# Optimization experiments

Measured on AMD Instinct MI355X. Metric: run time of the kernel, lower is better.

Reference implementation:

```python
import jax, jax.numpy as jnp
import numpy as np

SEGMENT_LENGTHS = (2048, 4096, 8192)
DILATION_RATES = (1, 2, 4)
NUM_HEADS = 12
EMBED_DIM = 768
B, N = 2, 8192


def setup_inputs() -> dict:
    key = jax.random.key(0)
    ks = jax.random.split(key, 11)
    E = EMBED_DIM
    return {
        "query": jax.random.normal(ks[0], (B, N, E), jnp.float32),
        "key": jax.random.normal(ks[1], (B, N, E), jnp.float32),
        "value": jax.random.normal(ks[2], (B, N, E), jnp.float32),
        "Wq": jax.random.normal(ks[3], (E, E), jnp.float32) * (E ** -0.5),
        "bq": jax.random.normal(ks[4], (E,), jnp.float32) * 0.02,
        "Wk": jax.random.normal(ks[5], (E, E), jnp.float32) * (E ** -0.5),
        "bk": jax.random.normal(ks[6], (E,), jnp.float32) * 0.02,
        "Wv": jax.random.normal(ks[7], (E, E), jnp.float32) * (E ** -0.5),
        "bv": jax.random.normal(ks[8], (E,), jnp.float32) * 0.02,
        "Wo": jax.random.normal(ks[9], (E, E), jnp.float32) * (E ** -0.5),
        "bo": jax.random.normal(ks[10], (E,), jnp.float32) * 0.02,
    }


def _dilated_attention(q, k, v):
    # q, k, v: [b, n, h, d]
    b, n, h, d = q.shape
    num_groups = len(DILATION_RATES)
    g = h // num_groups  # heads per dilation group
    scale = float(1.0 / np.sqrt(d))  # xformers default softmax scale
    out = jnp.zeros_like(q)
    for i, (r, s) in enumerate(zip(DILATION_RATES, SEGMENT_LENGTHS)):
        off = i % r
        hmin, hmax = i * g, (i + 1) * g
        nseg = n // s
        # gather: [b, nseg, s/r, g, d]
        qg = q.reshape(b, nseg, s, h, d)[:, :, off::r, hmin:hmax, :]
        kg = k.reshape(b, nseg, s, h, d)[:, :, off::r, hmin:hmax, :]
        vg = v.reshape(b, nseg, s, h, d)[:, :, off::r, hmin:hmax, :]
        scores = jnp.einsum("bnqhd,bnkhd->bnhqk", qg, kg) * scale
        attn = jax.nn.softmax(scores, axis=-1)
        x = jnp.einsum("bnhqk,bnkhd->bnqhd", attn, vg)
        out = (
            out.reshape(b, nseg, s, h, d)
            .at[:, :, off::r, hmin:hmax, :]
            .add(x)
            .reshape(b, n, h, d)
        )
    # faithful to original: normalize by sum over the sequence dimension
    return out / jnp.sum(out, axis=1, keepdims=True)


def reference(query, key, value, Wq, bq, Wk, bk, Wv, bv, Wo, bo):
    b, n, e = query.shape
    h = NUM_HEADS
    d = e // h
    q = (query @ Wq.T + bq).reshape(b, n, h, d)
    k = (key @ Wk.T + bk).reshape(b, n, h, d)
    v = (value @ Wv.T + bv).reshape(b, n, h, d)
    x = _dilated_attention(q, k, v)
    x = x.reshape(b, n, e)
    return x @ Wo.T + bo
```

## Files before the change

kernel.cpp:

```cpp
#include <hip/hip_runtime.h>
#include <hip/hip_bf16.h>
#include <cmath>
#include <cstdint>

#define B_ 2
#define N_ 8192
#define H_ 12
#define D_ 64
#define E_ 768
#define M_ (B_*N_)

typedef __attribute__((ext_vector_type(8))) short short8;
typedef __attribute__((ext_vector_type(4))) short short4v;
typedef __attribute__((ext_vector_type(4))) float float4v;

__device__ inline short f2b(float f) {
  union { float f; unsigned u; } x; x.f = f;
  unsigned r = (x.u + 0x7fffu + ((x.u >> 16) & 1u)) >> 16;
  return (short)r;
}
__device__ inline float b2f(short s) {
  union { unsigned u; float f; } x; x.u = ((unsigned)(unsigned short)s) << 16;
  return x.f;
}
__device__ inline void split2(float f, short& h, short& l) {
  h = f2b(f);
  l = f2b(f - b2f(h));
}
__device__ inline unsigned pack_trunc(float a, float b) {
  return (__float_as_uint(b) & 0xffff0000u) | (__float_as_uint(a) >> 16);
}

#define MFMA(a, b, c) __builtin_amdgcn_mfma_f32_16x16x32_bf16((a), (b), (c), 0, 0, 0)

#if __has_builtin(__builtin_amdgcn_mfma_f32_16x16x16_bf16)
#define MFMA16(a, b, c) __builtin_amdgcn_mfma_f32_16x16x16_bf16((a), (b), (c), 0, 0, 0)
#elif __has_builtin(__builtin_amdgcn_mfma_f32_16x16x16bf16_1k)
#define MFMA16(a, b, c) __builtin_amdgcn_mfma_f32_16x16x16bf16_1k((a), (b), (c), 0, 0, 0)
#else
__device__ inline float4v mfma16_asm(short4v a, short4v b, float4v c) {
  float4v d = c;
  asm volatile("v_mfma_f32_16x16x16_bf16 %0, %1, %2, %0"
               : "+v"(d) : "v"(a), "v"(b));
  return d;
}
#define MFMA16(a, b, c) mfma16_asm((a), (b), (c))
#endif

#define GLOAD_LDS16(g, l) \
  __builtin_amdgcn_global_load_lds((const __attribute__((address_space(1))) void*)(g), \
      (__attribute__((address_space(3))) void*)(l), 16, 0, 0)

__global__ __launch_bounds__(256) void split_kernel(const float* __restrict__ src,
    short* __restrict__ hi, short* __restrict__ lo, int count4)
{
  int i = blockIdx.x * 256 + threadIdx.x;
  if (i >= count4) return;
  float4v t = ((const float4v*)src)[i];
  short4v h4, l4; short hh, ll;
  split2(t.x, hh, ll); h4.x = hh; l4.x = ll;
  split2(t.y, hh, ll); h4.y = hh; l4.y = ll;
  split2(t.z, hh, ll); h4.z = hh; l4.z = ll;
  split2(t.w, hh, ll); h4.w = hh; l4.w = ll;
  ((short4v*)hi)[i] = h4;
  ((short4v*)lo)[i] = l4;
}

__global__ __launch_bounds__(256) void split_w4(
    const float* __restrict__ w0, const float* __restrict__ w1,
    const float* __restrict__ w2, const float* __restrict__ w3,
    short* __restrict__ planes)
{
  int which = blockIdx.y;
  const float* src = which == 0 ? w0 : which == 1 ? w1 : which == 2 ? w2 : w3;
  short* hi = planes + (size_t)(2 * which) * (E_ * E_);
  short* lo = planes + (size_t)(2 * which + 1) * (E_ * E_);
  int i = blockIdx.x * 256 + threadIdx.x;
  if (i >= E_ * E_ / 4) return;
  float4v t = ((const float4v*)src)[i];
  short4v h4, l4; short hh, ll;
  split2(t.x, hh, ll); h4.x = hh; l4.x = ll;
  split2(t.y, hh, ll); h4.y = hh; l4.y = ll;
  split2(t.z, hh, ll); h4.z = hh; l4.z = ll;
  split2(t.w, hh, ll); h4.w = hh; l4.w = ll;
  ((short4v*)hi)[i] = h4;
  ((short4v*)lo)[i] = l4;
}

__global__ __launch_bounds__(256) void inv_kernel(const float* __restrict__ sums,
    float* __restrict__ inv)
{
  int i = blockIdx.x * 256 + threadIdx.x;
  if (i < B_ * E_) inv[i] = 1.0f / sums[i];
}

__global__ __launch_bounds__(256) void prep_out(const float* __restrict__ attn,
    const float* __restrict__ inv, short* __restrict__ xnh, short* __restrict__ xnl)
{
  size_t e4 = ((size_t)blockIdx.x * 256 + threadIdx.x) * 4;
  int e = (int)(e4 % E_);
  int b = (int)(e4 / ((size_t)E_ * N_));
  float4v a = *(const float4v*)(attn + e4);
  float4v iv = *(const float4v*)(inv + (size_t)b * E_ + e);
  a *= iv;
  short4v h4, l4; short hh, ll;
  split2(a.x, hh, ll); h4.x = hh; l4.x = ll;
  split2(a.y, hh, ll); h4.y = hh; l4.y = ll;
  split2(a.z, hh, ll); h4.z = hh; l4.z = ll;
  split2(a.w, hh, ll); h4.w = hh; l4.w = ll;
  *(short4v*)&xnh[e4] = h4;
  *(short4v*)&xnl[e4] = l4;
}

template<bool OUT_PAIR>
__global__ __launch_bounds__(256) void gemm_dma(
    const short* __restrict__ Ah, const short* __restrict__ Al,
    const short* __restrict__ Wh, const short* __restrict__ Wl,
    const float* __restrict__ bias, void* __restrict__ OutH, short* __restrict__ OutL,
    float oscale)
{
  __shared__ short Ash[4096], Asl[4096], Wsh[4096], Wsl[4096];
  const int tid = threadIdx.x;
  const int m0 = blockIdx.y * 128;
  const int n0 = blockIdx.x * 128;
  const int w = tid >> 6, lane = tid & 63, quad = lane >> 4, l16 = lane & 15;
  const int wr = w >> 1, wc = w & 1;
  const int cq = (l16 >> 1) & 3;
  const int dmarow = lane >> 2;
  const int dmacc = (((lane & 3) ^ ((lane >> 3) & 3))) * 8;

  float4v acc[4][4];
#pragma unroll
  for (int a = 0; a < 4; ++a)
#pragma unroll
    for (int c = 0; c < 4; ++c) acc[a][c] = (float4v)0.0f;

  for (int kt = 0; kt < 24; ++kt) {
    const int k0 = kt * 32;
#pragma unroll
    for (int i = 0; i < 2; ++i) {
      int c = w * 2 + i;
      int ldso = c * 512 + lane * 8;
      size_t ga = (size_t)(m0 + c * 16 + dmarow) * E_ + k0 + dmacc;
      size_t gw = (size_t)(n0 + c * 16 + dmarow) * E_ + k0 + dmacc;
      GLOAD_LDS16(Ah + ga, &Ash[ldso]);
      GLOAD_LDS16(Al + ga, &Asl[ldso]);
      GLOAD_LDS16(Wh + gw, &Wsh[ldso]);
      GLOAD_LDS16(Wl + gw, &Wsl[ldso]);
    }
    __syncthreads();

    short8 afh[4], afl[4], bfh[4], bfl[4];
#pragma unroll
    for (int rt = 0; rt < 4; ++rt) {
      int ao = (wr * 64 + rt * 16 + l16) * 32 + (quad ^ cq) * 8;
      afh[rt] = *(const short8*)&Ash[ao];
      afl[rt] = *(const short8*)&Asl[ao];
      int wo = (wc * 64 + rt * 16 + l16) * 32 + (quad ^ cq) * 8;
      bfh[rt] = *(const short8*)&Wsh[wo];
      bfl[rt] = *(const short8*)&Wsl[wo];
    }
#pragma unroll
    for (int rt = 0; rt < 4; ++rt)
#pragma unroll
      for (int ct = 0; ct < 4; ++ct) {
        float4v a = acc[rt][ct];
        a = MFMA(afh[rt], bfh[ct], a);
        a = MFMA(afh[rt], bfl[ct], a);
        a = MFMA(afl[rt], bfh[ct], a);
        acc[rt][ct] = a;
      }
    __syncthreads();
  }

#pragma unroll
  for (int ct = 0; ct < 4; ++ct) {
    int n = n0 + wc * 64 + ct * 16 + l16;
    float bv = bias[n];
#pragma unroll
    for (int rt = 0; rt < 4; ++rt) {
#pragma unroll
      for (int i = 0; i < 4; ++i) {
        int m = m0 + wr * 64 + rt * 16 + quad * 4 + i;
        float v = (acc[rt][ct][i] + bv) * oscale;
        if constexpr (OUT_PAIR) {
          short hh, ll; split2(v, hh, ll);
          ((short*)OutH)[(size_t)m * E_ + n] = hh;
          OutL[(size_t)m * E_ + n] = ll;
        } else {
          ((float*)OutH)[(size_t)m * E_ + n] = v;
        }
      }
    }
  }
}

__device__ __host__ inline int hoff_of(int g, int hg) {
  return g == 0 ? hg * 8192 : (g == 1 ? 32768 + hg * 4096 : 49152 + hg * 2048);
}

__global__ __launch_bounds__(256) void transpose_v(const short* __restrict__ vh,
    const short* __restrict__ vl, short* __restrict__ vgh, short* __restrict__ vgl)
{
  __shared__ short Lh[64 * 68], Ll[64 * 68];
  int bid = blockIdx.x;
  int b = 0;
  if (bid >= 896) { b = 1; bid -= 896; }
  int g, hg, tile;
  if (bid < 512)      { g = 0; hg = bid >> 7; tile = bid & 127; }
  else if (bid < 768) { g = 1; hg = (bid - 512) >> 6; tile = (bid - 512) & 63; }
  else                { g = 2; hg = (bid - 768) >> 5; tile = (bid - 768) & 31; }
  const int h = g * 4 + hg, r = 1 << g, off = g;
  const int ext = 8192 >> g;
  const int jj0 = tile * 64, seg = jj0 >> 11, j0 = jj0 & 2047;
  const int n0 = seg * (2048 << g) + off + j0 * r;
  const int tid = threadIdx.x;

#pragma unroll
  for (int p = 0; p < 2; ++p) {
    int c = tid + p * 256;
    int jr = c >> 3, c8 = (c & 7) * 8;
    size_t gsrc = ((size_t)(b * N_ + n0 + jr * r) * H_ + h) * D_ + c8;
    *(short8*)&Lh[jr * 68 + c8] = *(const short8*)(vh + gsrc);
    *(short8*)&Ll[jr * 68 + c8] = *(const short8*)(vl + gsrc);
  }
  __syncthreads();
  size_t basebh = ((size_t)b * 57344 + hoff_of(g, hg)) * 64;
#pragma unroll
  for (int p = 0; p < 2; ++p) {
    int c = tid + p * 256;
    int dd = c >> 3, jc = (c & 7) * 8;
    short8 oh, ol;
#pragma unroll
    for (int u = 0; u < 8; ++u) {
      oh[u] = Lh[(jc + u) * 68 + dd];
      ol[u] = Ll[(jc + u) * 68 + dd];
    }
    size_t gdst = basebh + (size_t)dd * ext + jj0 + jc;
    *(short8*)(vgh + gdst) = oh;
    *(short8*)(vgl + gdst) = ol;
  }
}

__global__ __launch_bounds__(256, 4) void attn_kernel(
    const short* __restrict__ qh, const short* __restrict__ ql,
    const short* __restrict__ kh, const short* __restrict__ kl,
    const short* __restrict__ vgh, const short* __restrict__ vgl,
    float* __restrict__ attn_out, float* __restrict__ sums)
{
  __shared__ __align__(16) short Ksh[2][32 * 72], Ksl[2][32 * 72];
  __shared__ __align__(16) short Vth[2][64 * 40], Vtl[2][64 * 40];

  int bid = (blockIdx.x & 7) * 112 + (blockIdx.x >> 3);
  int g, t;
  if (bid < 512)      { g = 0; t = bid; }
  else if (bid < 768) { g = 1; t = bid - 512; }
  else                { g = 2; t = bid - 768; }
  const int qtile = t & 15; t >>= 4;
  const int hg = t & 3; t >>= 2;
  const int nseg = 4 >> g;
  const int seg = t & (nseg - 1);
  const int b = t / nseg;
  const int r = 1 << g;
  const int off = g;
  const int h = g * 4 + hg;
  const int segbase = seg * (2048 << g);
  const int ext = 8192 >> g;

  const int tid = threadIdx.x;
  const int w = tid >> 6, lane = tid & 63, quad = lane >> 4, l16 = lane & 15;

  const size_t vbase = ((size_t)b * 57344 + hoff_of(g, hg)) * 64 + (size_t)seg * 2048;

  if (g > 0) {
#pragma unroll
    for (int res0 = 1; res0 < 4; ++res0) {
      if (res0 >= r) break;
      int res = (off + res0) & (r - 1);
      for (int c = 0; c < 8; ++c) {
        int idx = tid + c * 256;
        int jl = idx >> 4, d0 = (idx & 15) * 4;
        int pos = segbase + res + (qtile * 128 + jl) * r;
        *(float4v*)(attn_out + ((size_t)(b * N_ + pos) * H_ + h) * D_ + d0) = (float4v)0.f;
      }
    }
  }

  short8 qfh[2][2], qfl[2][2];
#pragma unroll
  for (int qt = 0; qt < 2; ++qt) {
    int j = qtile * 128 + w * 32 + qt * 16 + l16;
    int pos = segbase + off + j * r;
    size_t base = ((size_t)(b * N_ + pos) * H_ + h) * D_;
#pragma unroll
    for (int ks = 0; ks < 2; ++ks) {
      qfh[qt][ks] = *(const short8*)(qh + base + ks * 32 + quad * 8);
      qfl[qt][ks] = *(const short8*)(ql + base + ks * 32 + quad * 8);
    }
  }

  const int srow = tid >> 3, sc8 = (tid & 7) * 8;
  const int sdd = tid >> 2, skvc = (tid & 3) * 8;
  size_t gbK = ((size_t)(b * N_ + segbase + off + srow * r) * H_ + h) * D_ + sc8;
  const size_t stepK = (size_t)32 * r * (H_ * D_);
  size_t gbV = vbase + (size_t)sdd * ext + skvc;

  short8 rkh, rkl, rvh, rvl;
#define LOADT(tt) do { \
    size_t ka_ = gbK + (size_t)(tt) * stepK; \
    size_t va_ = gbV + (size_t)(tt) * 32; \
    rkh = *(const short8*)(kh + ka_); rkl = *(const short8*)(kl + ka_); \
    rvh = *(const short8*)(vgh + va_); rvl = *(const short8*)(vgl + va_); \
  } while (0)
#define WRITET(cc) do { \
    *(short8*)&Ksh[cc][srow * 72 + sc8] = rkh; \
    *(short8*)&Ksl[cc][srow * 72 + sc8] = rkl; \
    *(short8*)&Vth[cc][sdd * 40 + skvc] = rvh; \
    *(short8*)&Vtl[cc][sdd * 40 + skvc] = rvl; \
  } while (0)

  float4v o[4][2];
  float mrow[2], lrow[2];
#pragma unroll
  for (int dt = 0; dt < 4; ++dt)
#pragma unroll
    for (int qt = 0; qt < 2; ++qt) o[dt][qt] = (float4v)0.0f;
  mrow[0] = mrow[1] = -INFINITY;
  lrow[0] = lrow[1] = 0.f;

  LOADT(0);
  WRITET(0);
  LOADT(1);
  __syncthreads();
  int cur = 0;

  for (int kt = 0; kt < 64; ++kt) {
    WRITET(cur ^ 1);
    LOADT((kt + 2) & 63);

    const short* Kc_h = Ksh[cur]; const short* Kc_l = Ksl[cur];
    const short* Vc_h = Vth[cur]; const short* Vc_l = Vtl[cur];

    float4v sc[2][2];
    __builtin_amdgcn_s_setprio(1);
#pragma unroll
    for (int kvt = 0; kvt < 2; ++kvt) {
      const int kb = (kvt * 16 + l16) * 72 + quad * 8;
      short8 ah0 = *(const short8*)&Kc_h[kb];
      short8 ah1 = *(const short8*)&Kc_h[kb + 32];
      short8 al0 = *(const short8*)&Kc_l[kb];
      short8 al1 = *(const short8*)&Kc_l[kb + 32];
#pragma unroll
      for (int qt = 0; qt < 2; ++qt) {
        float4v a = (float4v)0.0f;
        a = MFMA(ah0, qfh[qt][0], a); a = MFMA(ah1, qfh[qt][1], a);
        a = MFMA(ah0, qfl[qt][0], a); a = MFMA(ah1, qfl[qt][1], a);
        a = MFMA(al0, qfh[qt][0], a); a = MFMA(al1, qfh[qt][1], a);
        sc[qt][kvt] = a;
      }
    }
    __builtin_amdgcn_s_setprio(0);

    short4v pfh[2][2], pfl[2][2];
#pragma unroll
    for (int qt = 0; qt < 2; ++qt) {
      float mx = fmaxf(fmaxf(fmaxf(sc[qt][0][0], sc[qt][0][1]),
                             fmaxf(sc[qt][0][2], sc[qt][0][3])),
                       fmaxf(fmaxf(sc[qt][1][0], sc[qt][1][1]),
                             fmaxf(sc[qt][1][2], sc[qt][1][3])));
      mx = fmaxf(mx, __shfl_xor(mx, 16, 64));
      mx = fmaxf(mx, __shfl_xor(mx, 32, 64));
      if (__any(mx > mrow[qt] + 8.0f)) {
        float mnew = fmaxf(mrow[qt], mx);
        float alpha = exp2f(mrow[qt] - mnew);
        mrow[qt] = mnew;
        lrow[qt] *= alpha;
#pragma unroll
        for (int dt = 0; dt < 4; ++dt) o[dt][qt] *= alpha;
      }
      float rs = 0.f;
#pragma unroll
      for (int kvt = 0; kvt < 2; ++kvt) {
        float p0 = exp2f(sc[qt][kvt][0] - mrow[qt]);
        float p1 = exp2f(sc[qt][kvt][1] - mrow[qt]);
        float p2 = exp2f(sc[qt][kvt][2] - mrow[qt]);
        float p3 = exp2f(sc[qt][kvt][3] - mrow[qt]);
        rs += (p0 + p1) + (p2 + p3);
        union { unsigned u[2]; short4v s; } ph, pl;
        ph.u[0] = pack_trunc(p0, p1);
        ph.u[1] = pack_trunc(p2, p3);
        float l0 = p0 - __uint_as_float(__float_as_uint(p0) & 0xffff0000u);
        float l1 = p1 - __uint_as_float(__float_as_uint(p1) & 0xffff0000u);
        float l2 = p2 - __uint_as_float(__float_as_uint(p2) & 0xffff0000u);
        float l3 = p3 - __uint_as_float(__float_as_uint(p3) & 0xffff0000u);
        pl.u[0] = pack_trunc(l0, l1);
        pl.u[1] = pack_trunc(l2, l3);
        pfh[qt][kvt] = ph.s;
        pfl[qt][kvt] = pl.s;
      }
      lrow[qt] += rs;
    }

    __builtin_amdgcn_s_setprio(1);
#pragma unroll
    for (int dt = 0; dt < 4; ++dt) {
#pragma unroll
      for (int kvt = 0; kvt < 2; ++kvt) {
        const int vo = (dt * 16 + l16) * 40 + kvt * 16 + quad * 4;
        short4v vfh = *(const short4v*)&Vc_h[vo];
        short4v vfl = *(const short4v*)&Vc_l[vo];
#pragma unroll
        for (int qt = 0; qt < 2; ++qt) {
          float4v a = o[dt][qt];
          a = MFMA16(vfh, pfh[qt][kvt], a);
          a = MFMA16(vfh, pfl[qt][kvt], a);
          a = MFMA16(vfl, pfh[qt][kvt], a);
          o[dt][qt] = a;
        }
      }
    }
    __builtin_amdgcn_s_setprio(0);

    __syncthreads();
    cur ^= 1;
  }
#undef LOADT
#undef WRITET

  float4v sacc[4];
#pragma unroll
  for (int dt = 0; dt < 4; ++dt) sacc[dt] = (float4v)0.0f;
#pragma unroll
  for (int qt = 0; qt < 2; ++qt) {
    lrow[qt] += __shfl_xor(lrow[qt], 16, 64);
    lrow[qt] += __shfl_xor(lrow[qt], 32, 64);
    float inv_l = 1.0f / lrow[qt];
    int j = qtile * 128 + w * 32 + qt * 16 + l16;
    int pos = segbase + off + j * r;
    float* dst = attn_out + ((size_t)(b * N_ + pos) * H_ + h) * D_;
#pragma unroll
    for (int dt = 0; dt < 4; ++dt) {
      float4v v = o[dt][qt] * inv_l;
      *(float4v*)(dst + dt * 16 + quad * 4) = v;
      sacc[dt] += v;
    }
  }
#pragma unroll
  for (int dt = 0; dt < 4; ++dt) {
#pragma unroll
    for (int i = 0; i < 4; ++i) {
      float x = sacc[dt][i];
      x += __shfl_xor(x, 1, 64);
      x += __shfl_xor(x, 2, 64);
      x += __shfl_xor(x, 4, 64);
      x += __shfl_xor(x, 8, 64);
      if (l16 == 0)
        atomicAdd(&sums[(size_t)b * E_ + h * D_ + dt * 16 + quad * 4 + i], x);
    }
  }
}

extern "C" void kernel_launch(void* const* d_in, const int* in_sizes, int n_in,
                              void* d_out, int out_size, void* d_ws, size_t ws_size,
                              hipStream_t stream)
{
  const float* query = (const float*)d_in[0];
  const float* key_  = (const float*)d_in[1];
  const float* value = (const float*)d_in[2];
  const float* Wq = (const float*)d_in[3];
  const float* bq = (const float*)d_in[4];
  const float* Wk = (const float*)d_in[5];
  const float* bk = (const float*)d_in[6];
  const float* Wv = (const float*)d_in[7];
  const float* bv = (const float*)d_in[8];
  const float* Wo = (const float*)d_in[9];
  const float* bo = (const float*)d_in[10];

  char* ws = (char*)d_ws;
  const size_t szbf = (size_t)M_ * E_ * 2;
  const size_t szvg = (size_t)2 * 57344 * 64 * 2;
  const size_t szw  = (size_t)E_ * E_ * 2;
  short* qh_ = (short*)(ws);
  short* ql_ = (short*)(ws + 1 * szbf);
  short* kh_ = (short*)(ws + 2 * szbf);
  short* kl_ = (short*)(ws + 3 * szbf);
  short* vh_ = (short*)(ws + 4 * szbf);
  short* vl_ = (short*)(ws + 5 * szbf);
  short* ish = (short*)(ws + 6 * szbf);
  short* isl = (short*)(ws + 7 * szbf);
  short* vgh = (short*)(ws + 6 * szbf);
  short* vgl = (short*)(ws + 6 * szbf + szvg);
  short* wsp = (short*)(ws + 8 * szbf);
  float* sums = (float*)(ws + 8 * szbf + 8 * szw);
  float* attn = (float*)(ws + 4 * szbf);
  float* inv  = (float*)qh_;
  short* xnh = kh_;
  short* xnl = kl_;
  short* wqh = wsp + 0 * (szw / 2), *wql = wsp + 1 * (szw / 2);
  short* wkh = wsp + 2 * (szw / 2), *wkl = wsp + 3 * (szw / 2);
  short* wvh = wsp + 4 * (szw / 2), *wvl = wsp + 5 * (szw / 2);
  short* woh = wsp + 6 * (szw / 2), *wol = wsp + 7 * (szw / 2);

  hipMemsetAsync(sums, 0, (size_t)B_ * E_ * sizeof(float), stream);

  split_w4<<<dim3(576, 4), 256, 0, stream>>>(Wq, Wk, Wv, Wo, wsp);

  const int ac4 = M_ * E_ / 4;
  dim3 gg(6, 128), gb(256);
  const float qscale = 0.18033688f;
  split_kernel<<<12288, 256, 0, stream>>>(query, ish, isl, ac4);
  gemm_dma<true><<<gg, gb, 0, stream>>>(ish, isl, wqh, wql, bq, qh_, ql_, qscale);
  split_kernel<<<12288, 256, 0, stream>>>(key_, ish, isl, ac4);
  gemm_dma<true><<<gg, gb, 0, stream>>>(ish, isl, wkh, wkl, bk, kh_, kl_, 1.0f);
  split_kernel<<<12288, 256, 0, stream>>>(value, ish, isl, ac4);
  gemm_dma<true><<<gg, gb, 0, stream>>>(ish, isl, wvh, wvl, bv, vh_, vl_, 1.0f);

  transpose_v<<<1792, 256, 0, stream>>>(vh_, vl_, vgh, vgl);
  attn_kernel<<<896, 256, 0, stream>>>(qh_, ql_, kh_, kl_, vgh, vgl, attn, sums);
  inv_kernel<<<6, 256, 0, stream>>>(sums, inv);
  prep_out<<<12288, 256, 0, stream>>>(attn, inv, xnh, xnl);
  gemm_dma<false><<<gg, gb, 0, stream>>>(xnh, xnl, woh, wol, bo, d_out, nullptr, 1.0f);
}
```

Before: 850.6 us.

## Load K fragments directly to registers, swizzle V LDS, remap GEMM block order

```diff
diff --git a/kernel.cpp b/kernel.cpp
--- a/kernel.cpp
+++ b/kernel.cpp
@@ -121,8 +121,10 @@
 {
   __shared__ short Ash[4096], Asl[4096], Wsh[4096], Wsl[4096];
   const int tid = threadIdx.x;
-  const int m0 = blockIdx.y * 128;
-  const int n0 = blockIdx.x * 128;
+  const int flat = blockIdx.x + blockIdx.y * 6;
+  const int nid = (flat & 7) * 96 + (flat >> 3);
+  const int m0 = (nid / 6) * 128;
+  const int n0 = (nid % 6) * 128;
   const int w = tid >> 6, lane = tid & 63, quad = lane >> 4, l16 = lane & 15;
   const int wr = w >> 1, wc = w & 1;
   const int cq = (l16 >> 1) & 3;
@@ -242,14 +244,13 @@
   }
 }
 
-__global__ __launch_bounds__(256, 4) void attn_kernel(
+__global__ __launch_bounds__(256, 3) void attn_kernel(
     const short* __restrict__ qh, const short* __restrict__ ql,
     const short* __restrict__ kh, const short* __restrict__ kl,
     const short* __restrict__ vgh, const short* __restrict__ vgl,
     float* __restrict__ attn_out, float* __restrict__ sums)
 {
-  __shared__ __align__(16) short Ksh[2][32 * 72], Ksl[2][32 * 72];
-  __shared__ __align__(16) short Vth[2][64 * 40], Vtl[2][64 * 40];
+  __shared__ __align__(16) short Vth[2][64 * 32], Vtl[2][64 * 32];
 
   int bid = (blockIdx.x & 7) * 112 + (blockIdx.x >> 3);
   int g, t;
@@ -299,24 +300,37 @@
     }
   }
 
-  const int srow = tid >> 3, sc8 = (tid & 7) * 8;
-  const int sdd = tid >> 2, skvc = (tid & 3) * 8;
-  size_t gbK = ((size_t)(b * N_ + segbase + off + srow * r) * H_ + h) * D_ + sc8;
-  const size_t stepK = (size_t)32 * r * (H_ * D_);
-  size_t gbV = vbase + (size_t)sdd * ext + skvc;
-
-  short8 rkh, rkl, rvh, rvl;
-#define LOADT(tt) do { \
-    size_t ka_ = gbK + (size_t)(tt) * stepK; \
-    size_t va_ = gbV + (size_t)(tt) * 32; \
-    rkh = *(const short8*)(kh + ka_); rkl = *(const short8*)(kl + ka_); \
-    rvh = *(const short8*)(vgh + va_); rvl = *(const short8*)(vgl + va_); \
-  } while (0)
-#define WRITET(cc) do { \
-    *(short8*)&Ksh[cc][srow * 72 + sc8] = rkh; \
-    *(short8*)&Ksl[cc][srow * 72 + sc8] = rkl; \
-    *(short8*)&Vth[cc][sdd * 40 + skvc] = rvh; \
-    *(short8*)&Vtl[cc][sdd * 40 + skvc] = rvl; \
+  const int vd = tid >> 2;
+  const int vc = tid & 3;
+  const int vcc = vc ^ ((vd >> 1) & 3);
+  const bool vm0 = (vd & 1) != 0;
+  const int vldso = vd * 32 + vc * 8;
+  const int vrswz = l16 & 7;
+  size_t gbV = vbase + (size_t)vd * ext + vcc * 8;
+
+  size_t kbase = ((size_t)(b * N_ + segbase + off + l16 * r) * H_ + h) * D_ + quad * 8;
+  const size_t krstep = (size_t)r * (H_ * D_);
+
+  short8 rvh, rvl;
+  short8 kf_h[2][2], kf_l[2][2];
+#define LOADV(tt) do { size_t va_ = gbV + (size_t)(tt) * 32; \
+    rvh = *(const short8*)(vgh + va_); rvl = *(const short8*)(vgl + va_); } while (0)
+#define WRITEV(cc) do { \
+    short8 th_ = vm0 ? __builtin_shufflevector(rvh, rvh, 4, 5, 6, 7, 0, 1, 2, 3) : rvh; \
+    short8 tl_ = vm0 ? __builtin_shufflevector(rvl, rvl, 4, 5, 6, 7, 0, 1, 2, 3) : rvl; \
+    *(short8*)&Vth[cc][vldso] = th_; \
+    *(short8*)&Vtl[cc][vldso] = tl_; } while (0)
+#define KLOAD(tt) do { \
+    size_t ka_ = kbase + (size_t)((tt) * 32) * krstep; \
+    size_t kb_ = ka_ + 16 * krstep; \
+    kf_h[0][0] = *(const short8*)(kh + ka_); \
+    kf_h[0][1] = *(const short8*)(kh + ka_ + 32); \
+    kf_l[0][0] = *(const short8*)(kl + ka_); \
+    kf_l[0][1] = *(const short8*)(kl + ka_ + 32); \
+    kf_h[1][0] = *(const short8*)(kh + kb_); \
+    kf_h[1][1] = *(const short8*)(kh + kb_ + 32); \
+    kf_l[1][0] = *(const short8*)(kl + kb_); \
+    kf_l[1][1] = *(const short8*)(kl + kb_ + 32); \
   } while (0)
 
   float4v o[4][2];
@@ -328,38 +342,33 @@
   mrow[0] = mrow[1] = -INFINITY;
   lrow[0] = lrow[1] = 0.f;
 
-  LOADT(0);
-  WRITET(0);
-  LOADT(1);
+  LOADV(0);
+  WRITEV(0);
+  LOADV(1);
+  KLOAD(0);
   __syncthreads();
   int cur = 0;
 
   for (int kt = 0; kt < 64; ++kt) {
-    WRITET(cur ^ 1);
-    LOADT((kt + 2) & 63);
-
-    const short* Kc_h = Ksh[cur]; const short* Kc_l = Ksl[cur];
-    const short* Vc_h = Vth[cur]; const short* Vc_l = Vtl[cur];
+    WRITEV(cur ^ 1);
+    LOADV((kt + 2) & 63);
 
     float4v sc[2][2];
     __builtin_amdgcn_s_setprio(1);
 #pragma unroll
     for (int kvt = 0; kvt < 2; ++kvt) {
-      const int kb = (kvt * 16 + l16) * 72 + quad * 8;
-      short8 ah0 = *(const short8*)&Kc_h[kb];
-      short8 ah1 = *(const short8*)&Kc_h[kb + 32];
-      short8 al0 = *(const short8*)&Kc_l[kb];
-      short8 al1 = *(const short8*)&Kc_l[kb + 32];
 #pragma unroll
       for (int qt = 0; qt < 2; ++qt) {
         float4v a = (float4v)0.0f;
-        a = MFMA(ah0, qfh[qt][0], a); a = MFMA(ah1, qfh[qt][1], a);
-        a = MFMA(ah0, qfl[qt][0], a); a = MFMA(ah1, qfl[qt][1], a);
-        a = MFMA(al0, qfh[qt][0], a); a = MFMA(al1, qfh[qt][1], a);
+        a = MFMA(kf_h[kvt][0], qfh[qt][0], a); a = MFMA(kf_h[kvt][1], qfh[qt][1], a);
+        a = MFMA(kf_h[kvt][0], qfl[qt][0], a); a = MFMA(kf_h[kvt][1], qfl[qt][1], a);
+        a = MFMA(kf_l[kvt][0], qfh[qt][0], a); a = MFMA(kf_l[kvt][1], qfh[qt][1], a);
         sc[qt][kvt] = a;
       }
     }
     __builtin_amdgcn_s_setprio(0);
+
+    KLOAD((kt + 1) & 63);
 
     short4v pfh[2][2], pfl[2][2];
 #pragma unroll
@@ -402,20 +411,24 @@
     }
 
     __builtin_amdgcn_s_setprio(1);
-#pragma unroll
-    for (int dt = 0; dt < 4; ++dt) {
-#pragma unroll
-      for (int kvt = 0; kvt < 2; ++kvt) {
-        const int vo = (dt * 16 + l16) * 40 + kvt * 16 + quad * 4;
-        short4v vfh = *(const short4v*)&Vc_h[vo];
-        short4v vfl = *(const short4v*)&Vc_l[vo];
-#pragma unroll
-        for (int qt = 0; qt < 2; ++qt) {
-          float4v a = o[dt][qt];
-          a = MFMA16(vfh, pfh[qt][kvt], a);
-          a = MFMA16(vfh, pfl[qt][kvt], a);
-          a = MFMA16(vfl, pfh[qt][kvt], a);
-          o[dt][qt] = a;
+    {
+      const short* Vc_h = Vth[cur];
+      const short* Vc_l = Vtl[cur];
+#pragma unroll
+      for (int dt = 0; dt < 4; ++dt) {
+#pragma unroll
+        for (int kvt = 0; kvt < 2; ++kvt) {
+          const int vo = (dt * 16 + l16) * 32 + ((kvt * 4 + quad) ^ vrswz) * 4;
+          short4v vfh = *(const short4v*)&Vc_h[vo];
+          short4v vfl = *(const short4v*)&Vc_l[vo];
+#pragma unroll
+          for (int qt = 0; qt < 2; ++qt) {
+            float4v a = o[dt][qt];
+            a = MFMA16(vfh, pfh[qt][kvt], a);
+            a = MFMA16(vfh, pfl[qt][kvt], a);
+            a = MFMA16(vfl, pfh[qt][kvt], a);
+            o[dt][qt] = a;
+          }
         }
       }
     }
@@ -424,8 +437,9 @@
     __syncthreads();
     cur ^= 1;
   }
-#undef LOADT
-#undef WRITET
+#undef LOADV
+#undef WRITEV
+#undef KLOAD
 
   float4v sacc[4];
 #pragma unroll
```

After: 831.2 us. 1.02x faster.
